# Optimization experiments

Hardware: AMD Instinct MI355X
Metric: run time of the kernel (lower is better)

## Reference

```python
import jax, jax.numpy as jnp
import numpy as np

NUM_FILLERS = 50257
NUM_ROLES = 512
FILLER_DIM = 256  # D1
ROLE_DIM = 256    # D2
OUT_DIM = 1024
B, S = 64, 128


def setup_inputs() -> dict:
    key = jax.random.key(0)
    k1, k2, k3, k4, k5, k6 = jax.random.split(key, 6)
    fillers = jax.random.randint(k1, (B, S), 0, NUM_FILLERS)
    roles = jax.random.randint(k2, (B, S), 0, NUM_ROLES)
    filler_table = jax.random.normal(k3, (NUM_FILLERS, FILLER_DIM), dtype=jnp.float32)
    role_table = jax.random.normal(k4, (NUM_ROLES, ROLE_DIM), dtype=jnp.float32)
    # nn.Linear(filler_dim*role_dim, final_layer_width)
    lim = 1.0 / np.sqrt(FILLER_DIM * ROLE_DIM)
    W = jax.random.uniform(k5, (OUT_DIM, FILLER_DIM * ROLE_DIM), minval=-lim, maxval=lim, dtype=jnp.float32)
    b = jax.random.uniform(k6, (OUT_DIM,), minval=-lim, maxval=lim, dtype=jnp.float32)
    return {"fillers": fillers, "roles": roles, "filler_table": filler_table,
            "role_table": role_table, "W": W, "b": b}


def reference(fillers, roles, filler_table, role_table, W, b):
    # Embedding lookups: [B, S, D1] and [B, S, D2]
    f = filler_table[fillers]
    r = role_table[roles]
    # Sum over S of flattened outer products f_s (x) r_s -> [B, D1, D2]
    # (equivalent to the original's S*B rank-1 bmm + sum over S, fused as one GEMM)
    tp = jnp.einsum('bsd,bse->bde', f, r)
    tp = tp.reshape(f.shape[0], FILLER_DIM * ROLE_DIM)  # [B, D1*D2]
    # Final linear layer
    return tp @ W.T + b
```

## Files before the change

kernel.cpp:

```cpp
#include <hip/hip_runtime.h>
#include <hip/hip_bf16.h>

#define B_DIM 64
#define S_DIM 128
#define D1    256
#define D2    256
#define KTOT  65536
#define NOUT  1024

#define KSPLIT 64
#define KCHUNK (KTOT / KSPLIT)

typedef __attribute__((ext_vector_type(8))) short bf16x8;
typedef __attribute__((ext_vector_type(4))) float f32x4;

__device__ inline unsigned pack2bf16(float lo, float hi) {
    unsigned ulo = __float_as_uint(lo);
    unsigned uhi = __float_as_uint(hi);
    ulo = (ulo + 0x8000u) >> 16;
    uhi = (uhi + 0x8000u) & 0xffff0000u;
    return ulo | uhi;
}

__global__ __launch_bounds__(256) void bias_kernel(const float* __restrict__ bias,
                                                   float* __restrict__ out) {
    int i = blockIdx.x * 256 + threadIdx.x;
    out[i] = bias[i & (NOUT - 1)];
}

__global__ __launch_bounds__(256) void tp_kernel(const int* __restrict__ fillers,
                                                 const int* __restrict__ roles,
                                                 const float* __restrict__ ftab,
                                                 const float* __restrict__ rtab,
                                                 unsigned short* __restrict__ tp) {
    const int b     = blockIdx.x;
    const int dbase = blockIdx.y * 32;
    __shared__ float f_sh[S_DIM][32];
    __shared__ int   ridx[S_DIM];
    const int t = threadIdx.x;

    const int* fb = fillers + b * S_DIM;
    for (int i = t; i < S_DIM * 32; i += 256) {
        int s = i >> 5, dl = i & 31;
        f_sh[s][dl] = ftab[(long)fb[s] * D1 + dbase + dl];
    }
    if (t < S_DIM) ridx[t] = roles[b * S_DIM + t];
    __syncthreads();

    const int dsub = t >> 6;
    const int et   = t & 63;
    float acc[8][4];
#pragma unroll
    for (int i = 0; i < 8; ++i)
#pragma unroll
        for (int j = 0; j < 4; ++j) acc[i][j] = 0.f;

    for (int s = 0; s < S_DIM; ++s) {
        const float4 rv = *(const float4*)(rtab + ridx[s] * D2 + et * 4);
        const float4 f0 = *(const float4*)&f_sh[s][dsub * 8];
        const float4 f1 = *(const float4*)&f_sh[s][dsub * 8 + 4];
        float fv[8] = {f0.x, f0.y, f0.z, f0.w, f1.x, f1.y, f1.z, f1.w};
        float rr[4] = {rv.x, rv.y, rv.z, rv.w};
#pragma unroll
        for (int dl = 0; dl < 8; ++dl)
#pragma unroll
            for (int c = 0; c < 4; ++c) acc[dl][c] += fv[dl] * rr[c];
    }

    unsigned short* dst = tp + (size_t)b * KTOT + (size_t)(dbase + dsub * 8) * D2 + et * 4;
#pragma unroll
    for (int dl = 0; dl < 8; ++dl) {
        uint2 pp;
        pp.x = pack2bf16(acc[dl][0], acc[dl][1]);
        pp.y = pack2bf16(acc[dl][2], acc[dl][3]);
        *(uint2*)(dst + (size_t)dl * D2) = pp;
    }
}

__global__ __launch_bounds__(256) void gemm_kernel(const unsigned short* __restrict__ tp,
                                                   const float* __restrict__ W,
                                                   float* __restrict__ out) {
    const int nt  = blockIdx.x;
    const int ks  = blockIdx.y;
    const int w   = threadIdx.x >> 6;
    const int L   = threadIdx.x & 63;
    const int l16 = L & 15;
    const int lq  = L >> 4;
    const int ncol = nt * 64 + w * 16;
    const int k0   = ks * KCHUNK + lq * 8;

    const unsigned short* tpp = tp + (size_t)l16 * KTOT + k0;
    const float* wp = W + (size_t)(ncol + l16) * KTOT + k0;

    f32x4 acc[4];
#pragma unroll
    for (int mt = 0; mt < 4; ++mt) acc[mt] = (f32x4){0.f, 0.f, 0.f, 0.f};

#pragma unroll 4
    for (int kk = 0; kk < KCHUNK / 32; ++kk) {
        bf16x8 a0 = *(const bf16x8*)(tpp);
        bf16x8 a1 = *(const bf16x8*)(tpp + 16 * KTOT);
        bf16x8 a2 = *(const bf16x8*)(tpp + 32 * KTOT);
        bf16x8 a3 = *(const bf16x8*)(tpp + 48 * KTOT);
        float4 w0 = *(const float4*)wp;
        float4 w1 = *(const float4*)(wp + 4);
        int4 pb;
        pb.x = (int)pack2bf16(w0.x, w0.y);
        pb.y = (int)pack2bf16(w0.z, w0.w);
        pb.z = (int)pack2bf16(w1.x, w1.y);
        pb.w = (int)pack2bf16(w1.z, w1.w);
        bf16x8 bw = *(bf16x8*)&pb;
        acc[0] = __builtin_amdgcn_mfma_f32_16x16x32_bf16(a0, bw, acc[0], 0, 0, 0);
        acc[1] = __builtin_amdgcn_mfma_f32_16x16x32_bf16(a1, bw, acc[1], 0, 0, 0);
        acc[2] = __builtin_amdgcn_mfma_f32_16x16x32_bf16(a2, bw, acc[2], 0, 0, 0);
        acc[3] = __builtin_amdgcn_mfma_f32_16x16x32_bf16(a3, bw, acc[3], 0, 0, 0);
        tpp += 32;
        wp  += 32;
    }

#pragma unroll
    for (int mt = 0; mt < 4; ++mt)
#pragma unroll
        for (int r = 0; r < 4; ++r) {
            int row = mt * 16 + lq * 4 + r;
            atomicAdd(out + (size_t)row * NOUT + ncol + l16, acc[mt][r]);
        }
}

extern "C" void kernel_launch(void* const* d_in, const int* in_sizes, int n_in,
                              void* d_out, int out_size, void* d_ws, size_t ws_size,
                              hipStream_t stream) {
    const int*   fillers = (const int*)d_in[0];
    const int*   roles   = (const int*)d_in[1];
    const float* ftab    = (const float*)d_in[2];
    const float* rtab    = (const float*)d_in[3];
    const float* W       = (const float*)d_in[4];
    const float* bias    = (const float*)d_in[5];
    float* out = (float*)d_out;
    unsigned short* tp = (unsigned short*)d_ws;

    hipLaunchKernelGGL(bias_kernel, dim3(out_size / 256), dim3(256), 0, stream, bias, out);
    hipLaunchKernelGGL(tp_kernel, dim3(B_DIM, 8), dim3(256), 0, stream,
                       fillers, roles, ftab, rtab, tp);
    hipLaunchKernelGGL(gemm_kernel, dim3(16, KSPLIT), dim3(256), 0, stream, tp, W, out);
}
```

Baseline: 451.7 us.

## Replace atomic split-K reduction with partial buffers and separate reduce kernel

Doubles the K split to 128 chunks so more blocks run. Each block now writes its partial results to a workspace slice instead of issuing float atomics into the output. A new reduce kernel sums the slices and adds the bias, which replaces the bias-init kernel. The GEMM inner loop is fully unrolled with software prefetch of the next iteration's tp and W loads. This costs a 32 MB partial buffer write and read-back, plus a reduce launch that has only 64 blocks.

```diff
diff --git a/kernel.cpp b/kernel.cpp
--- a/kernel.cpp
+++ b/kernel.cpp
@@ -8,8 +8,9 @@
 #define KTOT  65536
 #define NOUT  1024
 
-#define KSPLIT 64
+#define KSPLIT 128
 #define KCHUNK (KTOT / KSPLIT)
+#define KITERS (KCHUNK / 32)
 
 typedef __attribute__((ext_vector_type(8))) short bf16x8;
 typedef __attribute__((ext_vector_type(4))) float f32x4;
@@ -20,12 +21,6 @@
     ulo = (ulo + 0x8000u) >> 16;
     uhi = (uhi + 0x8000u) & 0xffff0000u;
     return ulo | uhi;
-}
-
-__global__ __launch_bounds__(256) void bias_kernel(const float* __restrict__ bias,
-                                                   float* __restrict__ out) {
-    int i = blockIdx.x * 256 + threadIdx.x;
-    out[i] = bias[i & (NOUT - 1)];
 }
 
 __global__ __launch_bounds__(256) void tp_kernel(const int* __restrict__ fillers,
@@ -79,7 +74,7 @@
 
 __global__ __launch_bounds__(256) void gemm_kernel(const unsigned short* __restrict__ tp,
                                                    const float* __restrict__ W,
-                                                   float* __restrict__ out) {
+                                                   float* __restrict__ part) {
     const int nt  = blockIdx.x;
     const int ks  = blockIdx.y;
     const int w   = threadIdx.x >> 6;
@@ -90,41 +85,73 @@
     const int k0   = ks * KCHUNK + lq * 8;
 
     const unsigned short* tpp = tp + (size_t)l16 * KTOT + k0;
-    const float* wp = W + (size_t)(ncol + l16) * KTOT + k0;
+    const float*          wp  = W + (size_t)(ncol + l16) * KTOT + k0;
 
     f32x4 acc[4];
 #pragma unroll
     for (int mt = 0; mt < 4; ++mt) acc[mt] = (f32x4){0.f, 0.f, 0.f, 0.f};
 
-#pragma unroll 4
-    for (int kk = 0; kk < KCHUNK / 32; ++kk) {
-        bf16x8 a0 = *(const bf16x8*)(tpp);
-        bf16x8 a1 = *(const bf16x8*)(tpp + 16 * KTOT);
-        bf16x8 a2 = *(const bf16x8*)(tpp + 32 * KTOT);
-        bf16x8 a3 = *(const bf16x8*)(tpp + 48 * KTOT);
-        float4 w0 = *(const float4*)wp;
-        float4 w1 = *(const float4*)(wp + 4);
+    bf16x8 ca0 = *(const bf16x8*)(tpp);
+    bf16x8 ca1 = *(const bf16x8*)(tpp + 16 * KTOT);
+    bf16x8 ca2 = *(const bf16x8*)(tpp + 32 * KTOT);
+    bf16x8 ca3 = *(const bf16x8*)(tpp + 48 * KTOT);
+    float4 cw0 = *(const float4*)(wp);
+    float4 cw1 = *(const float4*)(wp + 4);
+
+#pragma unroll
+    for (int kk = 0; kk < KITERS; ++kk) {
+        bf16x8 na0, na1, na2, na3;
+        float4 nw0, nw1;
+        if (kk + 1 < KITERS) {
+            const unsigned short* tn = tpp + (kk + 1) * 32;
+            const float*          wn = wp + (kk + 1) * 32;
+            na0 = *(const bf16x8*)(tn);
+            na1 = *(const bf16x8*)(tn + 16 * KTOT);
+            na2 = *(const bf16x8*)(tn + 32 * KTOT);
+            na3 = *(const bf16x8*)(tn + 48 * KTOT);
+            nw0 = *(const float4*)(wn);
+            nw1 = *(const float4*)(wn + 4);
+        }
         int4 pb;
-        pb.x = (int)pack2bf16(w0.x, w0.y);
-        pb.y = (int)pack2bf16(w0.z, w0.w);
-        pb.z = (int)pack2bf16(w1.x, w1.y);
-        pb.w = (int)pack2bf16(w1.z, w1.w);
+        pb.x = (int)pack2bf16(cw0.x, cw0.y);
+        pb.y = (int)pack2bf16(cw0.z, cw0.w);
+        pb.z = (int)pack2bf16(cw1.x, cw1.y);
+        pb.w = (int)pack2bf16(cw1.z, cw1.w);
         bf16x8 bw = *(bf16x8*)&pb;
-        acc[0] = __builtin_amdgcn_mfma_f32_16x16x32_bf16(a0, bw, acc[0], 0, 0, 0);
-        acc[1] = __builtin_amdgcn_mfma_f32_16x16x32_bf16(a1, bw, acc[1], 0, 0, 0);
-        acc[2] = __builtin_amdgcn_mfma_f32_16x16x32_bf16(a2, bw, acc[2], 0, 0, 0);
-        acc[3] = __builtin_amdgcn_mfma_f32_16x16x32_bf16(a3, bw, acc[3], 0, 0, 0);
-        tpp += 32;
-        wp  += 32;
+        acc[0] = __builtin_amdgcn_mfma_f32_16x16x32_bf16(ca0, bw, acc[0], 0, 0, 0);
+        acc[1] = __builtin_amdgcn_mfma_f32_16x16x32_bf16(ca1, bw, acc[1], 0, 0, 0);
+        acc[2] = __builtin_amdgcn_mfma_f32_16x16x32_bf16(ca2, bw, acc[2], 0, 0, 0);
+        acc[3] = __builtin_amdgcn_mfma_f32_16x16x32_bf16(ca3, bw, acc[3], 0, 0, 0);
+        ca0 = na0; ca1 = na1; ca2 = na2; ca3 = na3;
+        cw0 = nw0; cw1 = nw1;
     }
 
+    float* pp = part + (size_t)ks * (B_DIM * NOUT) + ncol + l16;
 #pragma unroll
     for (int mt = 0; mt < 4; ++mt)
 #pragma unroll
-        for (int r = 0; r < 4; ++r) {
-            int row = mt * 16 + lq * 4 + r;
-            atomicAdd(out + (size_t)row * NOUT + ncol + l16, acc[mt][r]);
-        }
+        for (int r = 0; r < 4; ++r)
+            pp[(size_t)(mt * 16 + lq * 4 + r) * NOUT] = acc[mt][r];
+}
+
+__global__ __launch_bounds__(256) void reduce_kernel(const float* __restrict__ part,
+                                                     const float* __restrict__ bias,
+                                                     float* __restrict__ out) {
+    const int i    = blockIdx.x * 256 + threadIdx.x;
+    const size_t o = (size_t)i * 4;
+    const float* p = part + o;
+    f32x4 a0 = {0.f, 0.f, 0.f, 0.f};
+    f32x4 a1 = {0.f, 0.f, 0.f, 0.f};
+#pragma unroll 8
+    for (int ks = 0; ks < KSPLIT; ks += 2) {
+        f32x4 x = *(const f32x4*)(p + (size_t)ks * (B_DIM * NOUT));
+        f32x4 y = *(const f32x4*)(p + (size_t)(ks + 1) * (B_DIM * NOUT));
+        a0 += x;
+        a1 += y;
+    }
+    f32x4 bv = *(const f32x4*)(bias + (o & (NOUT - 1)));
+    f32x4 r  = a0 + a1 + bv;
+    *(f32x4*)(out + o) = r;
 }
 
 extern "C" void kernel_launch(void* const* d_in, const int* in_sizes, int n_in,
@@ -137,10 +164,12 @@
     const float* W       = (const float*)d_in[4];
     const float* bias    = (const float*)d_in[5];
     float* out = (float*)d_out;
-    unsigned short* tp = (unsigned short*)d_ws;
 
-    hipLaunchKernelGGL(bias_kernel, dim3(out_size / 256), dim3(256), 0, stream, bias, out);
+    float*          part = (float*)d_ws;
+    unsigned short* tp   = (unsigned short*)((char*)d_ws + (size_t)KSPLIT * B_DIM * NOUT * 4);
+
     hipLaunchKernelGGL(tp_kernel, dim3(B_DIM, 8), dim3(256), 0, stream,
                        fillers, roles, ftab, rtab, tp);
-    hipLaunchKernelGGL(gemm_kernel, dim3(16, KSPLIT), dim3(256), 0, stream, tp, W, out);
+    hipLaunchKernelGGL(gemm_kernel, dim3(16, KSPLIT), dim3(256), 0, stream, tp, W, part);
+    hipLaunchKernelGGL(reduce_kernel, dim3(64), dim3(256), 0, stream, part, bias, out);
 }
```

Result: no change. 453.2 us (+0.3%).
